# Kernel tuning notes

Measured on AMD Instinct MI355X. Metric: run time of the kernel, lower is better.

The kernel has to match this reference:

```python
import jax, jax.numpy as jnp
import numpy as np
import math

L, N, E, H = 2048, 4, 1024, 16  # seq_len, batch, embed_dim, num_heads
HD = E // H                      # head_dim = 64


def setup_inputs() -> dict:
    key = jax.random.key(0)
    ks = jax.random.split(key, 7)
    s = 1.0 / math.sqrt(E)
    return {
        "query": jax.random.normal(ks[0], (L, N, E), jnp.float32),
        "key": jax.random.normal(ks[1], (L, N, E), jnp.float32),
        "value": jax.random.normal(ks[2], (L, N, E), jnp.float32),
        "in_proj_weight": jax.random.normal(ks[3], (3 * E, E), jnp.float32) * s,
        "in_proj_bias": jax.random.normal(ks[4], (3 * E,), jnp.float32) * 0.02,
        "out_proj_weight": jax.random.normal(ks[5], (E, E), jnp.float32) * s,
        "out_proj_bias": jax.random.normal(ks[6], (E,), jnp.float32) * 0.02,
    }


def reference(query, key, value, in_proj_weight, in_proj_bias,
              out_proj_weight, out_proj_bias):
    # --- packed in-projection (q is k is v path of _in_projection_packed) ---
    # F.linear(x, W, b) = x @ W.T + b, W packed as [Wq; Wk; Wv] along dim 0.
    wq, wk, wv = jnp.split(in_proj_weight, 3, axis=0)   # each (E, E)
    bq, bk, bv = jnp.split(in_proj_bias, 3, axis=0)     # each (E,)
    q = query @ wq.T + bq   # (L, N, E)
    k = key @ wk.T + bk
    v = value @ wv.T + bv

    # --- split heads: (L, N, E) -> (N*H, L, HD), matching torch reshape/transpose ---
    def to_heads(x):
        return x.reshape(L, N * H, HD).transpose(1, 0, 2)
    q, k, v = to_heads(q), to_heads(k), to_heads(v)

    # --- scaled dot-product attention (q scaled by 1/sqrt(head_dim)) ---
    q = q / math.sqrt(HD)
    attn = jnp.einsum('bte,bse->bts', q, k)             # (N*H, L, L)
    attn = jax.nn.softmax(attn, axis=-1)
    out = jnp.einsum('bts,bse->bte', attn, v)           # (N*H, L, HD)

    # --- merge heads back to (L, N, E) ---
    out = out.transpose(1, 0, 2).reshape(L, N, E)

    # --- out-projection ---
    out = out @ out_proj_weight.T + out_proj_bias       # (L, N, E)
    return out
```

## Files before the change

### kernel.cpp

```cpp
#include <hip/hip_runtime.h>

using f16 = _Float16;
typedef _Float16 h8 __attribute__((ext_vector_type(8)));
typedef _Float16 h4 __attribute__((ext_vector_type(4)));
typedef float f32x4 __attribute__((ext_vector_type(4)));
typedef float f32x16 __attribute__((ext_vector_type(16)));
typedef unsigned u32x4 __attribute__((ext_vector_type(4)));

constexpr int L_SEQ  = 2048;
constexpr int NBATCH = 4;
constexpr int EMB    = 1024;
constexpr int NHEAD  = 16;
constexpr int HDIM   = 64;
constexpr int BH     = NBATCH * NHEAD;
constexpr int MROWS  = L_SEQ * NBATCH;

#define QSCALE (0.125f * 1.44269504088896341f)

__device__ __forceinline__ void glds16(const void* g, void* l) {
  __builtin_amdgcn_global_load_lds(
      (const __attribute__((address_space(1))) void*)g,
      (__attribute__((address_space(3))) void*)l, 16, 0, 0);
}

__device__ __forceinline__ f32x16 MFMA32(h8 a, h8 b, f32x16 c) {
  return __builtin_amdgcn_mfma_f32_32x32x16_f16(a, b, c, 0, 0, 0);
}
__device__ __forceinline__ unsigned pkrtz(float x, float y) {
  auto t = __builtin_amdgcn_cvt_pkrtz(x, y);
  return __builtin_bit_cast(unsigned, t);
}

__global__ __launch_bounds__(256)
void convert_w_kernel(const float* __restrict__ w, const float* __restrict__ wo,
                      f16* __restrict__ wb, f16* __restrict__ wob) {
  const int NW  = 3 * EMB * EMB / 4;
  const int NWO = EMB * EMB / 4;
  const int total = NW + NWO;
  int i = blockIdx.x * blockDim.x + threadIdx.x;
  const int stride = gridDim.x * blockDim.x;
  for (; i < total; i += stride) {
    const float* s; f16* d; int j;
    if (i < NW) { s = w;  d = wb;  j = i;      }
    else        { s = wo; d = wob; j = i - NW; }
    float4 t = reinterpret_cast<const float4*>(s)[j];
    h4 o = { (f16)t.x, (f16)t.y, (f16)t.z, (f16)t.w };
    reinterpret_cast<h4*>(d)[j] = o;
  }
}

__global__ __launch_bounds__(256)
void gemm_qkv(const float* __restrict__ qin, const float* __restrict__ kin,
              const float* __restrict__ vin, const f16* __restrict__ Btbase,
              const float* __restrict__ biasbase, f16* __restrict__ Hbase)
{
  const int id = blockIdx.x;
  const int x   = id & 7;
  const int bnI = (id >> 3) & 7;
  const int bmG = x + 8 * (id >> 6);
  const int z   = bmG >> 6;
  const int bm  = (bmG & 63) * 128;
  const int bn  = bnI * 128;

  const float* A = (z == 0) ? qin : (z == 1) ? kin : vin;
  const f16* Bt = Btbase + (size_t)z * EMB * EMB;
  const float* bias = biasbase + (size_t)z * EMB;

  const int t = threadIdx.x;
  const int w = t >> 6, lane = t & 63;
  const int wr = w >> 1, wc = w & 1;
  const int l16 = lane & 15, g = lane >> 4;

  __shared__ float Asf[2][128 * 32];
  __shared__ f16 Bs[2][128][32];

  f32x4 acc[4][4] = {};

  const int srow8 = lane >> 3;
  const int sslot = (lane & 7) ^ srow8;
  const float* gA = &A[(size_t)(bm + w*32 + srow8) * EMB + sslot * 4];

  const int sr  = lane >> 2;
  const int sc8 = (lane & 3) * 8;
  const f16* gB = &Bt[(size_t)(bn + w*32 + sr) * EMB + sc8];

#pragma unroll
  for (int r = 0; r < 4; ++r)
    glds16(gA + (size_t)r*8*EMB, &Asf[0][(w*32 + r*8) * 32]);
  glds16(gB, &Bs[0][w*32][0]);
  glds16(gB + (size_t)16*EMB, &Bs[0][w*32 + 16][0]);
  __syncthreads();

#pragma unroll 1
  for (int i = 0; i < 32; ++i) {
    const int cur = i & 1;
    if (i < 31) {
      const int k0 = (i + 1) * 32;
#pragma unroll
      for (int r = 0; r < 4; ++r)
        glds16(gA + (size_t)r*8*EMB + k0, &Asf[cur ^ 1][(w*32 + r*8) * 32]);
      glds16(gB + k0, &Bs[cur ^ 1][w*32][0]);
      glds16(gB + (size_t)16*EMB + k0, &Bs[cur ^ 1][w*32 + 16][0]);
    }

    h8 af[4], bfr[4];
#pragma unroll
    for (int m = 0; m < 4; ++m) {
      const int row = wr*64 + m*16 + l16;
      const int r7 = row & 7;
      f32x4 lo = *(const f32x4*)&Asf[cur][row*32 + (((g*2    ) ^ r7) << 2)];
      f32x4 hi = *(const f32x4*)&Asf[cur][row*32 + (((g*2 + 1) ^ r7) << 2)];
      u32x4 u = { pkrtz(lo[0], lo[1]), pkrtz(lo[2], lo[3]),
                  pkrtz(hi[0], hi[1]), pkrtz(hi[2], hi[3]) };
      af[m] = __builtin_bit_cast(h8, u);
    }
#pragma unroll
    for (int n = 0; n < 4; ++n) bfr[n] = *(const h8*)&Bs[cur][wc*64 + n*16 + l16][g*8];
    __builtin_amdgcn_s_setprio(1);
#pragma unroll
    for (int m = 0; m < 4; ++m)
#pragma unroll
      for (int n = 0; n < 4; ++n)
        acc[m][n] = __builtin_amdgcn_mfma_f32_16x16x32_f16(af[m], bfr[n], acc[m][n], 0, 0, 0);
    __builtin_amdgcn_s_setprio(0);
    __syncthreads();
  }

#pragma unroll
  for (int m = 0; m < 4; ++m) {
#pragma unroll
    for (int n = 0; n < 4; ++n) {
      const int col = bn + wc*64 + n*16 + l16;
      const float bv = bias[col];
#pragma unroll
      for (int r = 0; r < 4; ++r) {
        const int row = bm + wr*64 + m*16 + g*4 + r;
        float v = acc[m][n][r] + bv;
        if (z == 0) v *= QSCALE;
        const int l = row >> 2, nn = row & 3;
        const int h = col >> 6, hd = col & 63;
        Hbase[(((size_t)z * BH + nn * NHEAD + h) * L_SEQ + l) * HDIM + hd] = (f16)v;
      }
    }
  }
}

__global__ __launch_bounds__(256)
void gemm_out(const f16* __restrict__ A, const f16* __restrict__ Bt,
              const float* __restrict__ bias, float* __restrict__ Fout)
{
  const int id = blockIdx.x;
  const int x   = id & 7;
  const int bnI = (id >> 3) & 7;
  const int bmG = x + 8 * (id >> 6);
  const int bm  = bmG * 128;
  const int bn  = bnI * 128;

  const int t = threadIdx.x;
  const int w = t >> 6, lane = t & 63;
  const int wr = w >> 1, wc = w & 1;
  const int l16 = lane & 15, g = lane >> 4;

  __shared__ f16 As[2][128][32];
  __shared__ f16 Bs[2][128][32];

  f32x4 acc[4][4] = {};

  const int sr  = lane >> 2;
  const int sc8 = (lane & 3) * 8;
  const f16* gA = &A [(size_t)(bm + w*32 + sr) * EMB + sc8];
  const f16* gB = &Bt[(size_t)(bn + w*32 + sr) * EMB + sc8];

  glds16(gA, &As[0][w*32][0]);
  glds16(gA + (size_t)16*EMB, &As[0][w*32 + 16][0]);
  glds16(gB, &Bs[0][w*32][0]);
  glds16(gB + (size_t)16*EMB, &Bs[0][w*32 + 16][0]);
  __syncthreads();

#pragma unroll 1
  for (int i = 0; i < 32; ++i) {
    const int cur = i & 1;
    if (i < 31) {
      const int k0 = (i + 1) * 32;
      glds16(gA + k0, &As[cur ^ 1][w*32][0]);
      glds16(gA + (size_t)16*EMB + k0, &As[cur ^ 1][w*32 + 16][0]);
      glds16(gB + k0, &Bs[cur ^ 1][w*32][0]);
      glds16(gB + (size_t)16*EMB + k0, &Bs[cur ^ 1][w*32 + 16][0]);
    }

    h8 af[4], bfr[4];
#pragma unroll
    for (int m = 0; m < 4; ++m) af[m]  = *(const h8*)&As[cur][wr*64 + m*16 + l16][g*8];
#pragma unroll
    for (int n = 0; n < 4; ++n) bfr[n] = *(const h8*)&Bs[cur][wc*64 + n*16 + l16][g*8];
    __builtin_amdgcn_s_setprio(1);
#pragma unroll
    for (int m = 0; m < 4; ++m)
#pragma unroll
      for (int n = 0; n < 4; ++n)
        acc[m][n] = __builtin_amdgcn_mfma_f32_16x16x32_f16(af[m], bfr[n], acc[m][n], 0, 0, 0);
    __builtin_amdgcn_s_setprio(0);
    __syncthreads();
  }

#pragma unroll
  for (int m = 0; m < 4; ++m) {
#pragma unroll
    for (int n = 0; n < 4; ++n) {
      const int col = bn + wc*64 + n*16 + l16;
      const float bv = bias[col];
#pragma unroll
      for (int r = 0; r < 4; ++r) {
        const int row = bm + wr*64 + m*16 + g*4 + r;
        Fout[(size_t)row * EMB + col] = acc[m][n][r] + bv;
      }
    }
  }
}

__global__ __launch_bounds__(256)
void vtrans_kernel(const f16* __restrict__ V, f16* __restrict__ Vt) {
  const int b = blockIdx.y;
  const int t = threadIdx.x;
  const int d = t & 63;
  const int l0 = (blockIdx.x * 4 + (t >> 6)) * 8;
  const f16* Vb = V  + (size_t)b * L_SEQ * HDIM;
  f16* Vtb      = Vt + (size_t)b * L_SEQ * HDIM;
  h8 v;
#pragma unroll
  for (int i = 0; i < 8; ++i) v[i] = Vb[(size_t)(l0 + i) * HDIM + d];
  *(h8*)&Vtb[(size_t)d * L_SEQ + l0] = v;
}

__device__ __forceinline__ void attn11_step(
    const f16* __restrict__ Kc, const f16* __restrict__ Vc,
    const h8 (&qf)[4],
    f32x16 (&o)[2], float (&psum)[4],
    int l31, int hi)
{
  const int swz = (l31 & 7) << 3;

  h8 pa[4];
#pragma unroll
  for (int kt = 0; kt < 2; ++kt) {
    f32x16 acc = {};
    __builtin_amdgcn_s_setprio(1);
#pragma unroll
    for (int s = 0; s < 4; ++s) {
      h8 kf = *(const h8*)&Kc[(kt*32 + l31)*64 + ((s*16 + hi*8) ^ swz)];
      acc = MFMA32(kf, qf[s], acc);
    }
    __builtin_amdgcn_s_setprio(0);

#pragma unroll
    for (int half = 0; half < 2; ++half) {
      float p0 = __builtin_amdgcn_exp2f(acc[half*8+0]);
      float p1 = __builtin_amdgcn_exp2f(acc[half*8+1]);
      float p2 = __builtin_amdgcn_exp2f(acc[half*8+2]);
      float p3 = __builtin_amdgcn_exp2f(acc[half*8+3]);
      float p4 = __builtin_amdgcn_exp2f(acc[half*8+4]);
      float p5 = __builtin_amdgcn_exp2f(acc[half*8+5]);
      float p6 = __builtin_amdgcn_exp2f(acc[half*8+6]);
      float p7 = __builtin_amdgcn_exp2f(acc[half*8+7]);
      psum[0] += p0 + p4;
      psum[1] += p1 + p5;
      psum[2] += p2 + p6;
      psum[3] += p3 + p7;
      unsigned A = pkrtz(p0, p1);
      unsigned C = pkrtz(p2, p3);
      unsigned B = pkrtz(p4, p5);
      unsigned D = pkrtz(p6, p7);
      asm("v_permlane32_swap_b32 %0, %1" : "+v"(A), "+v"(B));
      asm("v_permlane32_swap_b32 %0, %1" : "+v"(C), "+v"(D));
      u32x4 wv = { A, C, B, D };
      pa[kt*2 + half] = __builtin_bit_cast(h8, wv);
    }
  }

#pragma unroll
  for (int s2 = 0; s2 < 4; ++s2) {
    h8 vf0 = *(const h8*)&Vc[(0*32 + l31)*64 + ((s2*16 + hi*8) ^ swz)];
    h8 vf1 = *(const h8*)&Vc[(1*32 + l31)*64 + ((s2*16 + hi*8) ^ swz)];
    __builtin_amdgcn_s_setprio(1);
    o[0] = MFMA32(pa[s2], vf0, o[0]);
    o[1] = MFMA32(pa[s2], vf1, o[1]);
    __builtin_amdgcn_s_setprio(0);
  }
}

__global__ __launch_bounds__(256, 4)
void attn11_kernel(const f16* __restrict__ Qh, const f16* __restrict__ Kh,
                   const f16* __restrict__ Vt, f16* __restrict__ AO)
{
  const int id = blockIdx.x;
  const int b    = (id & 7) | ((id >> 7) << 3);
  const int qblk = (id >> 3) & 15;

  const int t = threadIdx.x;
  const int w = t >> 6, lane = t & 63;
  const int l31 = lane & 31, hi = lane >> 5;

  const f16* Qb = Qh + (size_t)b * L_SEQ * HDIM;
  const f16* Kb = Kh + (size_t)b * L_SEQ * HDIM;
  const f16* Vb = Vt + (size_t)b * (size_t)HDIM * L_SEQ;

  __shared__ f16 Ks[2][64*64];
  __shared__ f16 Vs[2][64*64];

  const int q0 = qblk * 128 + w * 32;

  h8 qf[4];
#pragma unroll
  for (int s = 0; s < 4; ++s)
    qf[s] = *(const h8*)&Qb[(size_t)(q0 + l31) * HDIM + s*16 + hi*8];

  const int srow = lane >> 3;
  const int scol = 8 * ((lane & 7) ^ srow);
  const int r0   = w*16 + srow;
  const f16* gK0 = Kb + (size_t)(r0    ) * HDIM + scol;
  const f16* gK1 = Kb + (size_t)(r0 + 8) * HDIM + scol;
  const f16* gV0 = Vb + (size_t)(r0    ) * L_SEQ + scol;
  const f16* gV1 = Vb + (size_t)(r0 + 8) * L_SEQ + scol;
  const int ldsw = w * 1024;

  f32x16 o[2] = {};
  float psum[4] = { 0.f, 0.f, 0.f, 0.f };

  glds16(gK0, &Ks[0][ldsw]);
  glds16(gK1, &Ks[0][ldsw + 512]);
  glds16(gV0, &Vs[0][ldsw]);
  glds16(gV1, &Vs[0][ldsw + 512]);
  __syncthreads();

#pragma unroll 1
  for (int j0 = 0; j0 < L_SEQ; j0 += 128) {
    {
      const int jn = (j0 + 64) & (L_SEQ - 1);
      glds16(gK0 + (size_t)jn * HDIM, &Ks[1][ldsw]);
      glds16(gK1 + (size_t)jn * HDIM, &Ks[1][ldsw + 512]);
      glds16(gV0 + jn, &Vs[1][ldsw]);
      glds16(gV1 + jn, &Vs[1][ldsw + 512]);
      attn11_step(&Ks[0][0], &Vs[0][0], qf, o, psum, l31, hi);
      __syncthreads();
    }
    {
      const int jn = (j0 + 128) & (L_SEQ - 1);
      glds16(gK0 + (size_t)jn * HDIM, &Ks[0][ldsw]);
      glds16(gK1 + (size_t)jn * HDIM, &Ks[0][ldsw + 512]);
      glds16(gV0 + jn, &Vs[0][ldsw]);
      glds16(gV1 + jn, &Vs[0][ldsw + 512]);
      attn11_step(&Ks[1][0], &Vs[1][0], qf, o, psum, l31, hi);
      __syncthreads();
    }
  }

  float ssum = (psum[0] + psum[1]) + (psum[2] + psum[3]);
  ssum += __shfl_xor(ssum, 32);
  const float inv = 1.0f / ssum;

  const int nn = b >> 4, h = b & 15;
#pragma unroll
  for (int r = 0; r < 16; ++r) {
    const int qrow = (r & 3) + 8 * (r >> 2) + 4 * hi;
    const float iv = __shfl(inv, qrow);
    const int lr = q0 + qrow;
#pragma unroll
    for (int dt = 0; dt < 2; ++dt)
      AO[((size_t)lr * NBATCH + nn) * EMB + h*HDIM + dt*32 + l31] =
          (f16)(o[dt][r] * iv);
  }
}

extern "C" void kernel_launch(void* const* d_in, const int* in_sizes, int n_in,
                              void* d_out, int out_size, void* d_ws, size_t ws_size,
                              hipStream_t stream) {
  const float* query = (const float*)d_in[0];
  const float* key   = (const float*)d_in[1];
  const float* value = (const float*)d_in[2];
  const float* in_w  = (const float*)d_in[3];
  const float* in_b  = (const float*)d_in[4];
  const float* out_w = (const float*)d_in[5];
  const float* out_b = (const float*)d_in[6];
  float* out = (float*)d_out;

  char* ws = (char*)d_ws;
  size_t offH  = 0;
  size_t offX  = offH  + (size_t)3 * BH * L_SEQ * HDIM * 2;
  size_t offW  = offX  + (size_t)3 * MROWS * EMB * 2;
  size_t offWo = offW  + (size_t)3 * EMB * EMB * 2;
  size_t offAO = offWo + (size_t)EMB * EMB * 2;
  f16* Hbase = (f16*)(ws + offH);
  f16* Xb    = (f16*)(ws + offX);
  f16* Wb    = (f16*)(ws + offW);
  f16* Wob   = (f16*)(ws + offWo);
  f16* AOb   = (f16*)(ws + offAO);
  f16* Vtb   = Xb;

  hipLaunchKernelGGL(convert_w_kernel, dim3(1024), dim3(256), 0, stream,
                     in_w, out_w, Wb, Wob);

  hipLaunchKernelGGL(gemm_qkv, dim3(1536), dim3(256), 0, stream,
                     query, key, value, Wb, in_b, Hbase);

  f16* Vh = Hbase + (size_t)2 * BH * L_SEQ * HDIM;
  hipLaunchKernelGGL(vtrans_kernel, dim3(L_SEQ/32, BH), dim3(256), 0, stream, Vh, Vtb);

  hipLaunchKernelGGL(attn11_kernel, dim3(L_SEQ/128 * BH), dim3(256), 0, stream,
                     Hbase,
                     Hbase + (size_t)BH * L_SEQ * HDIM,
                     Vtb, AOb);

  hipLaunchKernelGGL(gemm_out, dim3(512), dim3(256), 0, stream,
                     AOb, Wob, out_b, out);
}
```

Before: 221.1 us.

## Triple-buffer the QKV projection GEMM with one barrier per k-step

The input-projection GEMM moves from double to triple buffering of the A and B shared-memory tiles, with two stages prefetched ahead. Each iteration waits with a partial vmcnt so only the current tile must have landed, then uses one barrier instead of a trailing __syncthreads. This is meant to hide global-to-LDS load latency better and remove one sync per k-step. The cost is 50% more LDS per block, which may lower occupancy.

```diff
diff --git a/kernel.cpp b/kernel.cpp
--- a/kernel.cpp
+++ b/kernel.cpp
@@ -71,8 +71,8 @@
   const int wr = w >> 1, wc = w & 1;
   const int l16 = lane & 15, g = lane >> 4;
 
-  __shared__ float Asf[2][128 * 32];
-  __shared__ f16 Bs[2][128][32];
+  __shared__ float Asf[3][128 * 32];
+  __shared__ f16 Bs[3][128][32];
 
   f32x4 acc[4][4] = {};
 
@@ -84,38 +84,28 @@
   const int sc8 = (lane & 3) * 8;
   const f16* gB = &Bt[(size_t)(bn + w*32 + sr) * EMB + sc8];
 
-#pragma unroll
-  for (int r = 0; r < 4; ++r)
-    glds16(gA + (size_t)r*8*EMB, &Asf[0][(w*32 + r*8) * 32]);
-  glds16(gB, &Bs[0][w*32][0]);
-  glds16(gB + (size_t)16*EMB, &Bs[0][w*32 + 16][0]);
-  __syncthreads();
-
-#pragma unroll 1
-  for (int i = 0; i < 32; ++i) {
-    const int cur = i & 1;
-    if (i < 31) {
-      const int k0 = (i + 1) * 32;
-#pragma unroll
-      for (int r = 0; r < 4; ++r)
-        glds16(gA + (size_t)r*8*EMB + k0, &Asf[cur ^ 1][(w*32 + r*8) * 32]);
-      glds16(gB + k0, &Bs[cur ^ 1][w*32][0]);
-      glds16(gB + (size_t)16*EMB + k0, &Bs[cur ^ 1][w*32 + 16][0]);
-    }
-
+  auto stage = [&](int buf, int k0) {
+#pragma unroll
+    for (int r = 0; r < 4; ++r)
+      glds16(gA + (size_t)r*8*EMB + k0, &Asf[buf][(w*32 + r*8) * 32]);
+    glds16(gB + k0, &Bs[buf][w*32][0]);
+    glds16(gB + (size_t)16*EMB + k0, &Bs[buf][w*32 + 16][0]);
+  };
+
+  auto compute = [&](int buf) {
     h8 af[4], bfr[4];
 #pragma unroll
     for (int m = 0; m < 4; ++m) {
       const int row = wr*64 + m*16 + l16;
       const int r7 = row & 7;
-      f32x4 lo = *(const f32x4*)&Asf[cur][row*32 + (((g*2    ) ^ r7) << 2)];
-      f32x4 hi = *(const f32x4*)&Asf[cur][row*32 + (((g*2 + 1) ^ r7) << 2)];
+      f32x4 lo = *(const f32x4*)&Asf[buf][row*32 + (((g*2    ) ^ r7) << 2)];
+      f32x4 hi = *(const f32x4*)&Asf[buf][row*32 + (((g*2 + 1) ^ r7) << 2)];
       u32x4 u = { pkrtz(lo[0], lo[1]), pkrtz(lo[2], lo[3]),
                   pkrtz(hi[0], hi[1]), pkrtz(hi[2], hi[3]) };
       af[m] = __builtin_bit_cast(h8, u);
     }
 #pragma unroll
-    for (int n = 0; n < 4; ++n) bfr[n] = *(const h8*)&Bs[cur][wc*64 + n*16 + l16][g*8];
+    for (int n = 0; n < 4; ++n) bfr[n] = *(const h8*)&Bs[buf][wc*64 + n*16 + l16][g*8];
     __builtin_amdgcn_s_setprio(1);
 #pragma unroll
     for (int m = 0; m < 4; ++m)
@@ -123,8 +113,30 @@
       for (int n = 0; n < 4; ++n)
         acc[m][n] = __builtin_amdgcn_mfma_f32_16x16x32_f16(af[m], bfr[n], acc[m][n], 0, 0, 0);
     __builtin_amdgcn_s_setprio(0);
-    __syncthreads();
-  }
+  };
+
+  stage(0, 0);
+  stage(1, 32);
+
+  int cur = 0;
+#pragma unroll 1
+  for (int i = 0; i < 31; ++i) {
+    asm volatile("s_waitcnt vmcnt(6)" ::: "memory");
+    __builtin_amdgcn_sched_barrier(0);
+    __builtin_amdgcn_s_barrier();
+    __builtin_amdgcn_sched_barrier(0);
+    if (i < 30) {
+      const int nb = (cur + 2 >= 3) ? cur - 1 : cur + 2;
+      stage(nb, (i + 2) * 32);
+    }
+    compute(cur);
+    cur = (cur == 2) ? 0 : cur + 1;
+  }
+  asm volatile("s_waitcnt vmcnt(0)" ::: "memory");
+  __builtin_amdgcn_sched_barrier(0);
+  __builtin_amdgcn_s_barrier();
+  __builtin_amdgcn_sched_barrier(0);
+  compute(cur);
 
 #pragma unroll
   for (int m = 0; m < 4; ++m) {
```

New measurement: 220.8 us. Within noise of the previous version (-0.1%).

## Pre-convert QKV activations to fp16 and swizzle GEMM LDS layout

Applied to the files above, without the earlier changes.

The fp32 query/key/value inputs are now converted to fp16 in a bulk conversion kernel, together with the weights. The QKV GEMM then loads fp16 A tiles instead of fp32 tiles with in-loop packing. Both GEMMs gain an XOR swizzle on LDS columns to reduce bank conflicts on fragment reads. The trade-off is an extra full pass over the activations (read 96MB fp32, write 48MB fp16) in exchange for halving the GEMM's A-tile LDS traffic and removing the conversion ALU work from its inner loop.

```diff
diff --git a/kernel.cpp b/kernel.cpp
--- a/kernel.cpp
+++ b/kernel.cpp
@@ -32,17 +32,24 @@
 }
 
 __global__ __launch_bounds__(256)
-void convert_w_kernel(const float* __restrict__ w, const float* __restrict__ wo,
-                      f16* __restrict__ wb, f16* __restrict__ wob) {
+void convert_all_kernel(const float* __restrict__ q, const float* __restrict__ k,
+                        const float* __restrict__ v, const float* __restrict__ w,
+                        const float* __restrict__ wo,
+                        f16* __restrict__ xq, f16* __restrict__ xk, f16* __restrict__ xv,
+                        f16* __restrict__ wb, f16* __restrict__ wob) {
+  const int NQ  = MROWS * EMB / 4;
   const int NW  = 3 * EMB * EMB / 4;
   const int NWO = EMB * EMB / 4;
-  const int total = NW + NWO;
+  const int total = 3 * NQ + NW + NWO;
   int i = blockIdx.x * blockDim.x + threadIdx.x;
   const int stride = gridDim.x * blockDim.x;
   for (; i < total; i += stride) {
     const float* s; f16* d; int j;
-    if (i < NW) { s = w;  d = wb;  j = i;      }
-    else        { s = wo; d = wob; j = i - NW; }
+    if      (i <     NQ)      { s = q;  d = xq;  j = i;              }
+    else if (i < 2 * NQ)      { s = k;  d = xk;  j = i - NQ;         }
+    else if (i < 3 * NQ)      { s = v;  d = xv;  j = i - 2 * NQ;     }
+    else if (i < 3 * NQ + NW) { s = w;  d = wb;  j = i - 3 * NQ;     }
+    else                      { s = wo; d = wob; j = i - 3 * NQ - NW; }
     float4 t = reinterpret_cast<const float4*>(s)[j];
     h4 o = { (f16)t.x, (f16)t.y, (f16)t.z, (f16)t.w };
     reinterpret_cast<h4*>(d)[j] = o;
@@ -50,8 +57,7 @@
 }
 
 __global__ __launch_bounds__(256)
-void gemm_qkv(const float* __restrict__ qin, const float* __restrict__ kin,
-              const float* __restrict__ vin, const f16* __restrict__ Btbase,
+void gemm_qkv(const f16* __restrict__ Abase, const f16* __restrict__ Btbase,
               const float* __restrict__ biasbase, f16* __restrict__ Hbase)
 {
   const int id = blockIdx.x;
@@ -62,7 +68,7 @@
   const int bm  = (bmG & 63) * 128;
   const int bn  = bnI * 128;
 
-  const float* A = (z == 0) ? qin : (z == 1) ? kin : vin;
+  const f16* A  = Abase  + (size_t)z * MROWS * EMB;
   const f16* Bt = Btbase + (size_t)z * EMB * EMB;
   const float* bias = biasbase + (size_t)z * EMB;
 
@@ -71,51 +77,40 @@
   const int wr = w >> 1, wc = w & 1;
   const int l16 = lane & 15, g = lane >> 4;
 
-  __shared__ float Asf[2][128 * 32];
+  __shared__ f16 As[2][128][32];
   __shared__ f16 Bs[2][128][32];
 
   f32x4 acc[4][4] = {};
 
-  const int srow8 = lane >> 3;
-  const int sslot = (lane & 7) ^ srow8;
-  const float* gA = &A[(size_t)(bm + w*32 + srow8) * EMB + sslot * 4];
-
   const int sr  = lane >> 2;
-  const int sc8 = (lane & 3) * 8;
+  const int sc8 = 8 * ((lane & 3) ^ ((lane >> 3) & 3));
+  const f16* gA = &A [(size_t)(bm + w*32 + sr) * EMB + sc8];
   const f16* gB = &Bt[(size_t)(bn + w*32 + sr) * EMB + sc8];
 
-#pragma unroll
-  for (int r = 0; r < 4; ++r)
-    glds16(gA + (size_t)r*8*EMB, &Asf[0][(w*32 + r*8) * 32]);
+  glds16(gA, &As[0][w*32][0]);
+  glds16(gA + (size_t)16*EMB, &As[0][w*32 + 16][0]);
   glds16(gB, &Bs[0][w*32][0]);
   glds16(gB + (size_t)16*EMB, &Bs[0][w*32 + 16][0]);
   __syncthreads();
+
+  const int fswz = (g ^ ((l16 >> 1) & 3)) * 8;
 
 #pragma unroll 1
   for (int i = 0; i < 32; ++i) {
     const int cur = i & 1;
     if (i < 31) {
       const int k0 = (i + 1) * 32;
-#pragma unroll
-      for (int r = 0; r < 4; ++r)
-        glds16(gA + (size_t)r*8*EMB + k0, &Asf[cur ^ 1][(w*32 + r*8) * 32]);
+      glds16(gA + k0, &As[cur ^ 1][w*32][0]);
+      glds16(gA + (size_t)16*EMB + k0, &As[cur ^ 1][w*32 + 16][0]);
       glds16(gB + k0, &Bs[cur ^ 1][w*32][0]);
       glds16(gB + (size_t)16*EMB + k0, &Bs[cur ^ 1][w*32 + 16][0]);
     }
 
     h8 af[4], bfr[4];
 #pragma unroll
-    for (int m = 0; m < 4; ++m) {
-      const int row = wr*64 + m*16 + l16;
-      const int r7 = row & 7;
-      f32x4 lo = *(const f32x4*)&Asf[cur][row*32 + (((g*2    ) ^ r7) << 2)];
-      f32x4 hi = *(const f32x4*)&Asf[cur][row*32 + (((g*2 + 1) ^ r7) << 2)];
-      u32x4 u = { pkrtz(lo[0], lo[1]), pkrtz(lo[2], lo[3]),
-                  pkrtz(hi[0], hi[1]), pkrtz(hi[2], hi[3]) };
-      af[m] = __builtin_bit_cast(h8, u);
-    }
-#pragma unroll
-    for (int n = 0; n < 4; ++n) bfr[n] = *(const h8*)&Bs[cur][wc*64 + n*16 + l16][g*8];
+    for (int m = 0; m < 4; ++m) af[m]  = *(const h8*)&As[cur][wr*64 + m*16 + l16][fswz];
+#pragma unroll
+    for (int n = 0; n < 4; ++n) bfr[n] = *(const h8*)&Bs[cur][wc*64 + n*16 + l16][fswz];
     __builtin_amdgcn_s_setprio(1);
 #pragma unroll
     for (int m = 0; m < 4; ++m)
@@ -167,7 +162,7 @@
   f32x4 acc[4][4] = {};
 
   const int sr  = lane >> 2;
-  const int sc8 = (lane & 3) * 8;
+  const int sc8 = 8 * ((lane & 3) ^ ((lane >> 3) & 3));
   const f16* gA = &A [(size_t)(bm + w*32 + sr) * EMB + sc8];
   const f16* gB = &Bt[(size_t)(bn + w*32 + sr) * EMB + sc8];
 
@@ -176,6 +171,8 @@
   glds16(gB, &Bs[0][w*32][0]);
   glds16(gB + (size_t)16*EMB, &Bs[0][w*32 + 16][0]);
   __syncthreads();
+
+  const int fswz = (g ^ ((l16 >> 1) & 3)) * 8;
 
 #pragma unroll 1
   for (int i = 0; i < 32; ++i) {
@@ -190,9 +187,9 @@
 
     h8 af[4], bfr[4];
 #pragma unroll
-    for (int m = 0; m < 4; ++m) af[m]  = *(const h8*)&As[cur][wr*64 + m*16 + l16][g*8];
-#pragma unroll
-    for (int n = 0; n < 4; ++n) bfr[n] = *(const h8*)&Bs[cur][wc*64 + n*16 + l16][g*8];
+    for (int m = 0; m < 4; ++m) af[m]  = *(const h8*)&As[cur][wr*64 + m*16 + l16][fswz];
+#pragma unroll
+    for (int n = 0; n < 4; ++n) bfr[n] = *(const h8*)&Bs[cur][wc*64 + n*16 + l16][fswz];
     __builtin_amdgcn_s_setprio(1);
 #pragma unroll
     for (int m = 0; m < 4; ++m)
@@ -396,11 +393,15 @@
   f16* AOb   = (f16*)(ws + offAO);
   f16* Vtb   = Xb;
 
-  hipLaunchKernelGGL(convert_w_kernel, dim3(1024), dim3(256), 0, stream,
-                     in_w, out_w, Wb, Wob);
+  hipLaunchKernelGGL(convert_all_kernel, dim3(2048), dim3(256), 0, stream,
+                     query, key, value, in_w, out_w,
+                     Xb + 0 * (size_t)MROWS * EMB,
+                     Xb + 1 * (size_t)MROWS * EMB,
+                     Xb + 2 * (size_t)MROWS * EMB,
+                     Wb, Wob);
 
   hipLaunchKernelGGL(gemm_qkv, dim3(1536), dim3(256), 0, stream,
-                     query, key, value, Wb, in_b, Hbase);
+                     Xb, Wb, in_b, Hbase);
 
   f16* Vh = Hbase + (size_t)2 * BH * L_SEQ * HDIM;
   hipLaunchKernelGGL(vtrans_kernel, dim3(L_SEQ/32, BH), dim3(256), 0, stream, Vh, Vtb);
```

Result: no change. 221.1 us (+0.0%).

## Convert activations to fp16 in registers before LDS and swizzle GEMM tiles

Applied to the files above, without the earlier changes.

The QKV projection kernel now loads fp32 activations into registers two steps ahead, packs them to fp16, and writes them to a half-size fp16 LDS tile. Before, it staged raw fp32 in LDS via global_load_lds and converted on every fragment read. An XOR swizzle is added to the LDS column slots of both GEMM kernels to avoid bank conflicts on fragment reads, and the loop is unrolled by two. The change cuts LDS footprint and repeated conversion work. In exchange it adds register pressure and synchronous global loads that the compiler must schedule around the MFMAs.

```diff
diff --git a/kernel.cpp b/kernel.cpp
--- a/kernel.cpp
+++ b/kernel.cpp
@@ -29,6 +29,11 @@
 __device__ __forceinline__ unsigned pkrtz(float x, float y) {
   auto t = __builtin_amdgcn_cvt_pkrtz(x, y);
   return __builtin_bit_cast(unsigned, t);
+}
+__device__ __forceinline__ h8 pack8(f32x4 a, f32x4 b) {
+  u32x4 u = { pkrtz(a[0], a[1]), pkrtz(a[2], a[3]),
+              pkrtz(b[0], b[1]), pkrtz(b[2], b[3]) };
+  return __builtin_bit_cast(h8, u);
 }
 
 __global__ __launch_bounds__(256)
@@ -71,51 +76,65 @@
   const int wr = w >> 1, wc = w & 1;
   const int l16 = lane & 15, g = lane >> 4;
 
-  __shared__ float Asf[2][128 * 32];
+  __shared__ f16 As[2][128][32];
   __shared__ f16 Bs[2][128][32];
 
   f32x4 acc[4][4] = {};
 
-  const int srow8 = lane >> 3;
-  const int sslot = (lane & 7) ^ srow8;
-  const float* gA = &A[(size_t)(bm + w*32 + srow8) * EMB + sslot * 4];
+  const int sr0 = lane >> 2;
+  const int sl  = lane & 3;
+  const float* gA = &A[(size_t)(bm + w*32 + sr0) * EMB + sl*8];
+  const int wslot = 8 * (sl ^ ((sr0 >> 1) & 3));
+  f16* lA0 = &As[0][w*32 + sr0][wslot];
+  f16* lA0b = &As[0][w*32 + 16 + sr0][wslot];
+  const int asStride = 128 * 32;
 
   const int sr  = lane >> 2;
-  const int sc8 = (lane & 3) * 8;
+  const int sc8 = 8 * ((lane & 3) ^ ((lane >> 3) & 3));
   const f16* gB = &Bt[(size_t)(bn + w*32 + sr) * EMB + sc8];
 
-#pragma unroll
-  for (int r = 0; r < 4; ++r)
-    glds16(gA + (size_t)r*8*EMB, &Asf[0][(w*32 + r*8) * 32]);
+  f32x4 ra0, ra1, rb0, rb1;
+  f32x4 sa0, sa1, sb0, sb1;
+
+  ra0 = *(const f32x4*)(gA);
+  ra1 = *(const f32x4*)(gA + 4);
+  rb0 = *(const f32x4*)(gA + (size_t)16*EMB);
+  rb1 = *(const f32x4*)(gA + (size_t)16*EMB + 4);
+  *(h8*)lA0  = pack8(ra0, ra1);
+  *(h8*)lA0b = pack8(rb0, rb1);
   glds16(gB, &Bs[0][w*32][0]);
   glds16(gB + (size_t)16*EMB, &Bs[0][w*32 + 16][0]);
+  sa0 = *(const f32x4*)(gA + 32);
+  sa1 = *(const f32x4*)(gA + 36);
+  sb0 = *(const f32x4*)(gA + (size_t)16*EMB + 32);
+  sb1 = *(const f32x4*)(gA + (size_t)16*EMB + 36);
+  glds16(gB + 32, &Bs[1][w*32][0]);
+  glds16(gB + (size_t)16*EMB + 32, &Bs[1][w*32 + 16][0]);
   __syncthreads();
 
-#pragma unroll 1
+  const int fswz = (g ^ ((l16 >> 1) & 3)) * 8;
+
+#pragma unroll 2
   for (int i = 0; i < 32; ++i) {
     const int cur = i & 1;
+    if (i < 30) {
+      const int k0 = (i + 2) * 32;
+      ra0 = *(const f32x4*)(gA + k0);
+      ra1 = *(const f32x4*)(gA + k0 + 4);
+      rb0 = *(const f32x4*)(gA + (size_t)16*EMB + k0);
+      rb1 = *(const f32x4*)(gA + (size_t)16*EMB + k0 + 4);
+    }
     if (i < 31) {
       const int k0 = (i + 1) * 32;
-#pragma unroll
-      for (int r = 0; r < 4; ++r)
-        glds16(gA + (size_t)r*8*EMB + k0, &Asf[cur ^ 1][(w*32 + r*8) * 32]);
       glds16(gB + k0, &Bs[cur ^ 1][w*32][0]);
       glds16(gB + (size_t)16*EMB + k0, &Bs[cur ^ 1][w*32 + 16][0]);
     }
 
     h8 af[4], bfr[4];
 #pragma unroll
-    for (int m = 0; m < 4; ++m) {
-      const int row = wr*64 + m*16 + l16;
-      const int r7 = row & 7;
-      f32x4 lo = *(const f32x4*)&Asf[cur][row*32 + (((g*2    ) ^ r7) << 2)];
-      f32x4 hi = *(const f32x4*)&Asf[cur][row*32 + (((g*2 + 1) ^ r7) << 2)];
-      u32x4 u = { pkrtz(lo[0], lo[1]), pkrtz(lo[2], lo[3]),
-                  pkrtz(hi[0], hi[1]), pkrtz(hi[2], hi[3]) };
-      af[m] = __builtin_bit_cast(h8, u);
-    }
-#pragma unroll
-    for (int n = 0; n < 4; ++n) bfr[n] = *(const h8*)&Bs[cur][wc*64 + n*16 + l16][g*8];
+    for (int m = 0; m < 4; ++m) af[m]  = *(const h8*)&As[cur][wr*64 + m*16 + l16][fswz];
+#pragma unroll
+    for (int n = 0; n < 4; ++n) bfr[n] = *(const h8*)&Bs[cur][wc*64 + n*16 + l16][fswz];
     __builtin_amdgcn_s_setprio(1);
 #pragma unroll
     for (int m = 0; m < 4; ++m)
@@ -123,6 +142,14 @@
       for (int n = 0; n < 4; ++n)
         acc[m][n] = __builtin_amdgcn_mfma_f32_16x16x32_f16(af[m], bfr[n], acc[m][n], 0, 0, 0);
     __builtin_amdgcn_s_setprio(0);
+
+    if (i < 31) {
+      f16* d0 = lA0  + (cur ^ 1) * asStride;
+      f16* d1 = lA0b + (cur ^ 1) * asStride;
+      *(h8*)d0 = pack8(sa0, sa1);
+      *(h8*)d1 = pack8(sb0, sb1);
+      sa0 = ra0; sa1 = ra1; sb0 = rb0; sb1 = rb1;
+    }
     __syncthreads();
   }
 
@@ -167,7 +194,7 @@
   f32x4 acc[4][4] = {};
 
   const int sr  = lane >> 2;
-  const int sc8 = (lane & 3) * 8;
+  const int sc8 = 8 * ((lane & 3) ^ ((lane >> 3) & 3));
   const f16* gA = &A [(size_t)(bm + w*32 + sr) * EMB + sc8];
   const f16* gB = &Bt[(size_t)(bn + w*32 + sr) * EMB + sc8];
 
@@ -176,6 +203,8 @@
   glds16(gB, &Bs[0][w*32][0]);
   glds16(gB + (size_t)16*EMB, &Bs[0][w*32 + 16][0]);
   __syncthreads();
+
+  const int fswz = (g ^ ((l16 >> 1) & 3)) * 8;
 
 #pragma unroll 1
   for (int i = 0; i < 32; ++i) {
@@ -190,9 +219,9 @@
 
     h8 af[4], bfr[4];
 #pragma unroll
-    for (int m = 0; m < 4; ++m) af[m]  = *(const h8*)&As[cur][wr*64 + m*16 + l16][g*8];
-#pragma unroll
-    for (int n = 0; n < 4; ++n) bfr[n] = *(const h8*)&Bs[cur][wc*64 + n*16 + l16][g*8];
+    for (int m = 0; m < 4; ++m) af[m]  = *(const h8*)&As[cur][wr*64 + m*16 + l16][fswz];
+#pragma unroll
+    for (int n = 0; n < 4; ++n) bfr[n] = *(const h8*)&Bs[cur][wc*64 + n*16 + l16][fswz];
     __builtin_amdgcn_s_setprio(1);
 #pragma unroll
     for (int m = 0; m < 4; ++m)
```

New measurement: 212.6 us (median of 2 runs). -3.8%, faster.
